# Performance work log

Measured on AMD Instinct MI355X. Metric: run time of the kernel, lower is better.

## Reference

```python
import jax, jax.numpy as jnp
import numpy as np

D_MODEL = 1024
N_HEADS = 16
HEAD_DIM = D_MODEL // N_HEADS
NEG_INF = -1e30


def _rotary(v):
    # v: [B, H, T, hd]. Original module rotates each (even, odd) pair by 90 deg:
    # out[..., 2i] = -v[..., 2i+1]; out[..., 2i+1] = v[..., 2i]
    v2 = v.reshape(*v.shape[:-1], HEAD_DIM // 2, 2)
    return jnp.stack([-v2[..., 1], v2[..., 0]], axis=-1).reshape(v.shape)


def setup_inputs() -> dict:
    key = jax.random.key(0)
    ks = jax.random.split(key, 9)
    B, T, D = 2, 2048, D_MODEL
    s = 1.0 / np.sqrt(D)
    inp = {
        "x": jax.random.normal(ks[0], (B, T, D), dtype=jnp.float32),
        "Wq_w": jax.random.normal(ks[1], (D, D), dtype=jnp.float32) * s,
        "Wq_b": jnp.zeros((D,), dtype=jnp.float32),
        "Wk_w": jax.random.normal(ks[2], (D, D), dtype=jnp.float32) * s,
        "Wk_b": jnp.zeros((D,), dtype=jnp.float32),
        "Wv_w": jax.random.normal(ks[3], (D, D), dtype=jnp.float32) * s,
        "Wv_b": jnp.zeros((D,), dtype=jnp.float32),
        "Wo_w": jax.random.normal(ks[4], (D, D), dtype=jnp.float32) * s,
        "Wo_b": jnp.zeros((D,), dtype=jnp.float32),
    }
    # create_sparse_mask: block-diagonal True windows of size T//4
    window = T // 4
    blk = jnp.arange(T) // window
    inp["sparse_mask"] = blk[:, None] == blk[None, :]
    return inp


def reference(x, Wq_w, Wq_b, Wk_w, Wk_b, Wv_w, Wv_b, Wo_w, Wo_b, sparse_mask):
    B, T, D = x.shape
    H, hd = N_HEADS, HEAD_DIM

    def proj(w, b):  # [B,T,D] -> [B,H,T,hd]
        return (x @ w.T + b).reshape(B, T, H, hd).transpose(0, 2, 1, 3)

    q = _rotary(proj(Wq_w, Wq_b))
    k = _rotary(proj(Wk_w, Wk_b))
    v = proj(Wv_w, Wv_b)

    scores = jnp.einsum("bhqd,bhkd->bhqk", q, k) / jnp.sqrt(jnp.asarray(hd, x.dtype))
    causal = jnp.tril(jnp.ones((T, T), dtype=bool))
    allowed = sparse_mask & causal  # block-diagonal AND causal
    scores = jnp.where(allowed, scores, NEG_INF)
    attn = jax.nn.softmax(scores, axis=-1)  # dropout_p=0.1 omitted (eval mode)
    out = jnp.einsum("bhqk,bhkd->bhqd", attn, v)
    out = out.transpose(0, 2, 1, 3).reshape(B, T, D)
    return out @ Wo_w.T + Wo_b
```

## Files before the change

### kernel.cpp

```cpp
#include <hip/hip_runtime.h>
#include <hip/hip_bf16.h>
#include <stdint.h>

typedef __attribute__((ext_vector_type(4))) float f32x4;
typedef __attribute__((ext_vector_type(8))) __bf16 bf16x8;
typedef __attribute__((ext_vector_type(4))) unsigned short u16x4;
typedef __attribute__((ext_vector_type(8))) unsigned short u16x8;
typedef __attribute__((ext_vector_type(2))) unsigned int u32x2;
typedef const __attribute__((address_space(1))) void* as1_cvp;
typedef __attribute__((address_space(3))) void* as3_vp;

#define LOG2E 1.44269504088896340736f

#define VMW0() asm volatile("s_waitcnt vmcnt(0)" ::: "memory")
#define VMW2() asm volatile("s_waitcnt vmcnt(2)" ::: "memory")
#define VMW4() asm volatile("s_waitcnt vmcnt(4)" ::: "memory")
#define BAR()  do { __builtin_amdgcn_sched_barrier(0); __builtin_amdgcn_s_barrier(); \
                    __builtin_amdgcn_sched_barrier(0); } while (0)

static __device__ __forceinline__ unsigned short f2bf(float f) {
  union { float f; unsigned int u; } c; c.f = f;
  unsigned int r = c.u + 0x7FFFu + ((c.u >> 16) & 1u);
  return (unsigned short)(r >> 16);
}

static __device__ __forceinline__ void gl_lds16(const void* g, void* l) {
  __builtin_amdgcn_global_load_lds((as1_cvp)(uintptr_t)g, (as3_vp)(uintptr_t)l, 16, 0, 0);
}

__global__ __launch_bounds__(256) void cvt_kernel(
    const float* __restrict__ x, const float* __restrict__ wq, const float* __restrict__ wk,
    const float* __restrict__ wv, const float* __restrict__ wo,
    unsigned short* __restrict__ xb, unsigned short* __restrict__ wqb,
    unsigned short* __restrict__ wkb, unsigned short* __restrict__ wvb,
    unsigned short* __restrict__ wob) {
  long e = ((long)blockIdx.x * 256 + threadIdx.x) * 8;
  const float* s; unsigned short* d; long o;
  if (e < 4194304)      { s = x;  d = xb;  o = e; }
  else if (e < 5242880) { s = wq; d = wqb; o = e - 4194304; }
  else if (e < 6291456) { s = wk; d = wkb; o = e - 5242880; }
  else if (e < 7340032) { s = wv; d = wvb; o = e - 6291456; }
  else                  { s = wo; d = wob; o = e - 7340032; }
  float4 a = *(const float4*)(s + o);
  float4 b = *(const float4*)(s + o + 4);
  u16x8 v;
  v[0] = f2bf(a.x); v[1] = f2bf(a.y); v[2] = f2bf(a.z); v[3] = f2bf(a.w);
  v[4] = f2bf(b.x); v[5] = f2bf(b.y); v[6] = f2bf(b.z); v[7] = f2bf(b.w);
  *(u16x8*)(d + o) = v;
}

__global__ __launch_bounds__(512, 2) void gemm_qkv8(
    const unsigned short* __restrict__ xb, const unsigned short* __restrict__ wcat,
    const float* __restrict__ bq, const float* __restrict__ bk, const float* __restrict__ bv,
    unsigned short* __restrict__ qo, unsigned short* __restrict__ ko,
    unsigned short* __restrict__ vto) {
  __shared__ __align__(16) char lds[114688];
  const int tid = threadIdx.x;
  const int lane = tid & 63, wid = tid >> 6;
  const int wm = wid >> 1, wn = wid & 1;
  const int c = lane & 15, g = lane >> 4;

  const int bid = blockIdx.x;
  const int xcd = bid & 7, idx = bid >> 3;
  const int m0 = (((xcd >> 1) << 2) + (idx >> 3)) << 8;
  const int n0 = (((xcd & 1) << 3) + (idx & 7)) * 192;

  const int srow = tid >> 3;
  const int coff = (((tid & 7) ^ (srow & 7)) << 4);
  const char* Ab = (const char*)xb;
  const char* Bb = (const char*)wcat;

  const int swzr0 = ((g ^ (c & 7)) << 4);
  const int swzr1 = (((4 | g) ^ (c & 7)) << 4);

  f32x4 acc[4][6] = {};

  auto STAGE = [&](int kt, int unit) {
    char* db = lds + (kt & 1) * 57344;
    const char* gp; char* dst;
    if (unit < 3) {
      gp = Bb + ((long)(n0 + unit * 64 + srow) << 11) + (kt << 7) + coff;
      dst = db + 32768 + unit * 8192 + tid * 16;
    } else {
      const int u = unit - 3;
      gp = Ab + ((long)(m0 + u * 64 + srow) << 11) + (kt << 7) + coff;
      dst = db + u * 8192 + tid * 16;
    }
    gl_lds16(gp, dst);
  };

#pragma unroll
  for (int uu = 0; uu < 7; ++uu) STAGE(0, uu);
  VMW0();
  BAR();

#pragma unroll 1
  for (int kt = 0; kt < 16; ++kt) {
    const int bufb = (kt & 1) * 57344;
    if (kt < 15) {
#pragma unroll
      for (int uu = 0; uu < 7; ++uu) STAGE(kt + 1, uu);
    }
    bf16x8 aa[4][2];
    const char* pA = lds + bufb + (wm << 13) + (c << 7);
#pragma unroll
    for (int f = 0; f < 4; ++f) {
      aa[f][0] = *(const bf16x8*)(pA + (f << 11) + swzr0);
      aa[f][1] = *(const bf16x8*)(pA + (f << 11) + swzr1);
    }
#pragma unroll
    for (int nf = 0; nf < 6; ++nf) {
      const int rB = wn * 96 + (nf << 4) + c;
      const char* pB = lds + bufb + 32768 + ((rB >> 6) << 13) + ((rB & 63) << 7);
      bf16x8 b0 = *(const bf16x8*)(pB + swzr0);
      bf16x8 b1 = *(const bf16x8*)(pB + swzr1);
      __builtin_amdgcn_s_setprio(1);
#pragma unroll
      for (int f = 0; f < 4; ++f)
        acc[f][nf] = __builtin_amdgcn_mfma_f32_16x16x32_bf16(aa[f][0], b0, acc[f][nf], 0, 0, 0);
#pragma unroll
      for (int f = 0; f < 4; ++f)
        acc[f][nf] = __builtin_amdgcn_mfma_f32_16x16x32_bf16(aa[f][1], b1, acc[f][nf], 0, 0, 0);
      __builtin_amdgcn_s_setprio(0);
    }
    if (kt < 15) VMW0();
    BAR();
  }

#pragma unroll
  for (int nf = 0; nf < 6; ++nf) {
    const int n = n0 + wn * 96 + (nf << 4) + c;
    const int z = n >> 10, nn = n & 1023;
    const float bb_ = (z == 0 ? bq : z == 1 ? bk : bv)[nn];
    const float sc = (z == 0) ? 0.125f : 1.0f;
    const int h = nn >> 6, dd = nn & 63;
#pragma unroll
    for (int a = 0; a < 4; ++a) {
      const int mb = m0 + (wm << 6) + (a << 4) + (g << 2);
      const int b = mb >> 11, tt = mb & 2047;
      if (z < 2) {
        unsigned short* dst = (z == 0 ? qo : ko) +
            ((((long)(b << 4) + h) << 11) + tt) * 64 + dd;
#pragma unroll
        for (int j = 0; j < 4; ++j) dst[(long)j * 64] = f2bf((acc[a][nf][j] + bb_) * sc);
      } else {
        u16x4 pk;
#pragma unroll
        for (int j = 0; j < 4; ++j) pk[j] = f2bf(acc[a][nf][j] + bb_);
        *(u16x4*)(vto + ((((long)((b << 4) + h) << 6) + dd) << 11) + tt) = pk;
      }
    }
  }
}

__global__ __launch_bounds__(512, 2) void gemm_oproj8(
    const unsigned short* __restrict__ ab, const unsigned short* __restrict__ wob,
    const float* __restrict__ bo, float* __restrict__ out) {
  __shared__ __align__(16) char lds[65536];
  const int tid = threadIdx.x;
  const int lane = tid & 63, wid = tid >> 6;
  const int wm = wid >> 2, wn = wid & 3;
  const int c = lane & 15, g = lane >> 4;

  const int bid = blockIdx.x;
  const int swz = (bid & 7) * 32 + (bid >> 3);
  const int n0 = (swz & 7) << 7;
  const int m0 = (swz >> 3) << 7;

  const int srow = tid >> 3;
  const int coff = (((tid & 7) ^ (srow & 7)) << 4);
  const char* Ab = (const char*)ab;
  const char* Bb = (const char*)wob;

  const int swzr0 = ((g ^ (c & 7)) << 4);
  const int swzr1 = (((4 | g) ^ (c & 7)) << 4);

  f32x4 acc[4][2] = {};
  bf16x8 afrA[2][2], afrB[2][2], bbf[2][2];

  auto STAGE = [&](int kt, int unit) {
    char* db = lds + (kt & 1) * 32768;
    const char* gp;
    if (unit < 2) gp = Ab + ((long)(m0 + unit * 64 + srow) << 11) + (kt << 7) + coff;
    else          gp = Bb + ((long)(n0 + (unit - 2) * 64 + srow) << 11) + (kt << 7) + coff;
    gl_lds16(gp, db + unit * 8192 + tid * 16);
  };
  auto RDA = [&](bf16x8 (&dst)[2][2], int bufb, int u) {
    const char* p = lds + bufb + (((u << 6) + (wm << 5) + c) << 7);
#pragma unroll
    for (int f = 0; f < 2; ++f) {
      dst[f][0] = *(const bf16x8*)(p + (f << 11) + swzr0);
      dst[f][1] = *(const bf16x8*)(p + (f << 11) + swzr1);
    }
  };
  auto RDB = [&](int bufb) {
#pragma unroll
    for (int nf = 0; nf < 2; ++nf) {
      const char* p = lds + bufb + 16384 + (((nf << 6) + (wn << 4) + c) << 7);
      bbf[nf][0] = *(const bf16x8*)(p + swzr0);
      bbf[nf][1] = *(const bf16x8*)(p + swzr1);
    }
  };
  auto MM = [&](int u, const bf16x8 (&af)[2][2]) {
    __builtin_amdgcn_s_setprio(1);
#pragma unroll
    for (int f = 0; f < 2; ++f)
#pragma unroll
      for (int nf = 0; nf < 2; ++nf)
#pragma unroll
        for (int kf = 0; kf < 2; ++kf)
          acc[u * 2 + f][nf] = __builtin_amdgcn_mfma_f32_16x16x32_bf16(
              af[f][kf], bbf[nf][kf], acc[u * 2 + f][nf], 0, 0, 0);
    __builtin_amdgcn_s_setprio(0);
  };

  STAGE(0, 0); STAGE(0, 2); STAGE(0, 3); STAGE(0, 1);

#pragma unroll 1
  for (int kt = 0; kt < 15; ++kt) {
    const int bufb = (kt & 1) * 32768;
    STAGE(kt + 1, 0); STAGE(kt + 1, 2);
    VMW2(); BAR();
    RDB(bufb); RDA(afrA, bufb, 0); RDA(afrB, bufb, 1);
    MM(0, afrA);
    STAGE(kt + 1, 3); STAGE(kt + 1, 1);
    BAR();
    MM(1, afrB);
  }
  {
    VMW0(); BAR();
    RDB(32768); RDA(afrA, 32768, 0); RDA(afrB, 32768, 1);
    MM(0, afrA);
    MM(1, afrB);
  }

#pragma unroll
  for (int nf = 0; nf < 2; ++nf) {
    const int n = n0 + (nf << 6) + (wn << 4) + c;
    const float bb = bo[n];
#pragma unroll
    for (int a = 0; a < 4; ++a) {
      const int mb = m0 + ((a >> 1) << 6) + (wm << 5) + ((a & 1) << 4) + (g << 2);
#pragma unroll
      for (int j = 0; j < 4; ++j)
        out[((long)(mb + j) << 10) + n] = acc[a][nf][j] + bb;
    }
  }
}

__global__ __launch_bounds__(512) void attn_kernel(
    const unsigned short* __restrict__ qg, const unsigned short* __restrict__ kg,
    const unsigned short* __restrict__ vtg, unsigned short* __restrict__ og) {
  __shared__ __align__(16) char kv_s[3][16384];
  __shared__ __align__(16) char p_s[8][2304];

  const int bx = blockIdx.x, bh = blockIdx.y;
  const int map1[16] = {3,7,11,15, 2,6,10,14, 0,4,8,12, 1,5,9,13};
  const int map2[16] = {0,4,8,12, 1,5,9,13, 3,7,11,15, 2,6,10,14};
  const int qt = (bh < 16) ? map1[bx] : map2[bx];
  const int tid = threadIdx.x;
  const int lane = tid & 63, w = tid >> 6;
  const int c = lane & 15, g = lane >> 4;
  const int q0 = qt << 7;
  const int wstart = q0 & ~511;
  const int nt = ((q0 - wstart) >> 6) + 2;

  const unsigned short* qrow = qg + (((long)bh << 11) + q0 + (w << 4) + c) * 64;
  bf16x8 qa0 = *(const bf16x8*)(qrow + (g << 3));
  bf16x8 qa1 = *(const bf16x8*)(qrow + (g << 3) + 32);

  float m_run = -3.0e38f, l_run = 0.0f;
  f32x4 oacc[4] = {};

  const int sr = tid >> 3;
  const int jx16 = (((tid & 7) ^ (sr & 7)) << 4);
  const char* kbase = (const char*)kg + ((((long)bh << 11) + sr) << 7) + jx16;
  const char* vbase = (const char*)vtg + ((((long)bh << 6) + sr) << 12) + jx16;
  const int t16 = tid << 4;

  auto STAGEKV = [&](int kv0, int bsel) {
    char* dst = kv_s[bsel];
    gl_lds16(kbase + ((long)kv0 << 7), dst + t16);
    gl_lds16(vbase + ((long)kv0 << 1), dst + 8192 + t16);
  };

  STAGEKV(wstart, 0);
  STAGEKV(wstart + 64, 1);

  int rsel = 0, ssel = 2;
  for (int t = 0; t < nt; ++t) {
    if (t + 2 < nt) {
      STAGEKV(wstart + ((t + 2) << 6), ssel);
      VMW4();
    } else if (t + 1 < nt) {
      VMW2();
    } else {
      VMW0();
    }
    BAR();

    const char* kb_ = kv_s[rsel];
    const char* vb_ = kv_s[rsel] + 8192;
    const int kv0 = wstart + (t << 6);

    f32x4 sacc[4] = {};
    __builtin_amdgcn_s_setprio(1);
#pragma unroll
    for (int mf = 0; mf < 4; ++mf) {
      const int kr = (mf << 4) + c;
      const char* kp = kb_ + (kr << 7);
      bf16x8 k0 = *(const bf16x8*)(kp + ((g ^ (kr & 7)) << 4));
      bf16x8 k1 = *(const bf16x8*)(kp + (((4 | g) ^ (kr & 7)) << 4));
      sacc[mf] = __builtin_amdgcn_mfma_f32_16x16x32_bf16(k0, qa0, sacc[mf], 0, 0, 0);
      sacc[mf] = __builtin_amdgcn_mfma_f32_16x16x32_bf16(k1, qa1, sacc[mf], 0, 0, 0);
    }
    __builtin_amdgcn_s_setprio(0);

    const int dkv = kv0 - q0;
    if (dkv > (w << 4) - 64) {
      const int qrel = (w << 4) + c;
#pragma unroll
      for (int mf = 0; mf < 4; ++mf)
#pragma unroll
        for (int j = 0; j < 4; ++j)
          if (dkv + (mf << 4) + (g << 2) + j > qrel) sacc[mf][j] = -3.0e38f;
    }

    float pm[4];
#pragma unroll
    for (int mf = 0; mf < 4; ++mf)
      pm[mf] = fmaxf(fmaxf(sacc[mf][0], sacc[mf][1]), fmaxf(sacc[mf][2], sacc[mf][3]));
    float pmax = fmaxf(fmaxf(pm[0], pm[1]), fmaxf(pm[2], pm[3]));
    pmax = fmaxf(pmax, __shfl_xor(pmax, 16));
    pmax = fmaxf(pmax, __shfl_xor(pmax, 32));

    const bool resc = !__all(pmax <= m_run + 8.0f);
    const float m_new = resc ? fmaxf(m_run, pmax) : m_run;

    const float mL = m_new * LOG2E;
    float ls[4];
#pragma unroll
    for (int mf = 0; mf < 4; ++mf) {
      float p0 = __builtin_amdgcn_exp2f(__builtin_fmaf(sacc[mf][0], LOG2E, -mL));
      float p1 = __builtin_amdgcn_exp2f(__builtin_fmaf(sacc[mf][1], LOG2E, -mL));
      float p2 = __builtin_amdgcn_exp2f(__builtin_fmaf(sacc[mf][2], LOG2E, -mL));
      float p3 = __builtin_amdgcn_exp2f(__builtin_fmaf(sacc[mf][3], LOG2E, -mL));
      sacc[mf][0] = p0; sacc[mf][1] = p1; sacc[mf][2] = p2; sacc[mf][3] = p3;
      ls[mf] = (p0 + p1) + (p2 + p3);
    }
    float lsum = (ls[0] + ls[1]) + (ls[2] + ls[3]);
    lsum += __shfl_xor(lsum, 16);
    lsum += __shfl_xor(lsum, 32);

    if (resc) {
      const float alpha = __builtin_amdgcn_exp2f((m_run - m_new) * LOG2E);
      l_run *= alpha;
#pragma unroll
      for (int j = 0; j < 4; ++j) {
        const float aj = __shfl(alpha, (g << 2) + j);
#pragma unroll
        for (int nf = 0; nf < 4; ++nf) oacc[nf][j] *= aj;
      }
      m_run = m_new;
    }
    l_run += lsum;

    {
      char* pw = p_s[w] + c * 144;
#pragma unroll
      for (int mf = 0; mf < 4; ++mf) {
        unsigned int p01, p23;
        asm("v_cvt_pk_bf16_f32 %0, %1, %2" : "=v"(p01) : "v"(sacc[mf][0]), "v"(sacc[mf][1]));
        asm("v_cvt_pk_bf16_f32 %0, %1, %2" : "=v"(p23) : "v"(sacc[mf][2]), "v"(sacc[mf][3]));
        u32x2 pk; pk[0] = p01; pk[1] = p23;
        *(u32x2*)(pw + (mf << 5) + (g << 3)) = pk;
      }
    }

    const char* pr = p_s[w] + c * 144;
    __builtin_amdgcn_s_setprio(1);
#pragma unroll
    for (int kk = 0; kk < 2; ++kk) {
      bf16x8 pa = *(const bf16x8*)(pr + (kk << 6) + (g << 4));
#pragma unroll
      for (int nf = 0; nf < 4; ++nf) {
        const int vr = (nf << 4) + c;
        bf16x8 vb = *(const bf16x8*)(vb_ + (vr << 7) +
                                     ((((kk << 2) | g) ^ (vr & 7)) << 4));
        oacc[nf] = __builtin_amdgcn_mfma_f32_16x16x32_bf16(pa, vb, oacc[nf], 0, 0, 0);
      }
    }
    __builtin_amdgcn_s_setprio(0);
    BAR();

    rsel = (rsel == 2) ? 0 : rsel + 1;
    ssel = (ssel == 2) ? 0 : ssel + 1;
  }

  const int b = bh >> 4, h = bh & 15;
#pragma unroll
  for (int j = 0; j < 4; ++j) {
    const float linv = 1.0f / __shfl(l_run, (g << 2) + j);
    const int trow = q0 + (w << 4) + (g << 2) + j;
    unsigned short* dst = og + ((((long)(b << 11)) + trow) << 10) + (h << 6);
#pragma unroll
    for (int nf = 0; nf < 4; ++nf)
      dst[(nf << 4) + c] = f2bf(oacc[nf][j] * linv);
  }
}

extern "C" void kernel_launch(void* const* d_in, const int* in_sizes, int n_in,
                              void* d_out, int out_size, void* d_ws, size_t ws_size,
                              hipStream_t stream) {
  const float* x  = (const float*)d_in[0];
  const float* wq = (const float*)d_in[1];
  const float* bq = (const float*)d_in[2];
  const float* wk = (const float*)d_in[3];
  const float* bk = (const float*)d_in[4];
  const float* wv = (const float*)d_in[5];
  const float* bv = (const float*)d_in[6];
  const float* wo = (const float*)d_in[7];
  const float* bo = (const float*)d_in[8];

  char* ws = (char*)d_ws;
  unsigned short* xb    = (unsigned short*)(ws);
  unsigned short* wqb   = (unsigned short*)(ws + 8388608);
  unsigned short* wkb   = (unsigned short*)(ws + 10485760);
  unsigned short* wvb   = (unsigned short*)(ws + 12582912);
  unsigned short* wob   = (unsigned short*)(ws + 14680064);
  unsigned short* qb    = (unsigned short*)(ws + 16777216);
  unsigned short* kb    = (unsigned short*)(ws + 25165824);
  unsigned short* vtb   = (unsigned short*)(ws + 33554432);
  unsigned short* attnb = xb;

  cvt_kernel<<<4096, 256, 0, stream>>>(x, wq, wk, wv, wo, xb, wqb, wkb, wvb, wob);
  gemm_qkv8<<<256, 512, 0, stream>>>(xb, wqb, bq, bk, bv, qb, kb, vtb);
  attn_kernel<<<dim3(16, 32), 512, 0, stream>>>(qb, kb, vtb, attnb);
  gemm_oproj8<<<256, 512, 0, stream>>>(attnb, wob, bo, (float*)d_out);
}
```

Measured before the change: 77.98 us.

## Halve GEMM tile sizes to double grid size and raise occupancy

Both the QKV and output-projection GEMMs shrink their M tile (256→128 and 128→64 rows), so each launches 512 blocks instead of 256 and uses less LDS with fewer accumulators, allowing four blocks per CU. The output projection also drops its split-stage software pipeline in favor of the simpler double-buffered loop used by the QKV kernel, and both get new XCD-aware block-to-tile mappings. The aim is to fill all CUs better on a small problem. The cost is less data reuse per block (more global/LDS traffic per FLOP) and the loss of the finer-grained overlap in oproj.

Result: faster. 72.38 us (-7.2%).

```diff
diff --git a/kernel.cpp b/kernel.cpp
--- a/kernel.cpp
+++ b/kernel.cpp
@@ -49,20 +49,20 @@
   *(u16x8*)(d + o) = v;
 }
 
-__global__ __launch_bounds__(512, 2) void gemm_qkv8(
+__global__ __launch_bounds__(512, 4) void gemm_qkv8(
     const unsigned short* __restrict__ xb, const unsigned short* __restrict__ wcat,
     const float* __restrict__ bq, const float* __restrict__ bk, const float* __restrict__ bv,
     unsigned short* __restrict__ qo, unsigned short* __restrict__ ko,
     unsigned short* __restrict__ vto) {
-  __shared__ __align__(16) char lds[114688];
+  __shared__ __align__(16) char lds[81920];
   const int tid = threadIdx.x;
   const int lane = tid & 63, wid = tid >> 6;
-  const int wm = wid >> 1, wn = wid & 1;
+  const int wm = wid >> 2, wn = wid & 3;
   const int c = lane & 15, g = lane >> 4;
 
   const int bid = blockIdx.x;
   const int xcd = bid & 7, idx = bid >> 3;
-  const int m0 = (((xcd >> 1) << 2) + (idx >> 3)) << 8;
+  const int m0 = (((xcd >> 1) << 3) + (idx >> 3)) << 7;
   const int n0 = (((xcd & 1) << 3) + (idx & 7)) * 192;
 
   const int srow = tid >> 3;
@@ -73,33 +73,32 @@
   const int swzr0 = ((g ^ (c & 7)) << 4);
   const int swzr1 = (((4 | g) ^ (c & 7)) << 4);
 
-  f32x4 acc[4][6] = {};
+  f32x4 acc[4][3] = {};
 
   auto STAGE = [&](int kt, int unit) {
-    char* db = lds + (kt & 1) * 57344;
+    char* db = lds + (kt & 1) * 40960;
     const char* gp; char* dst;
-    if (unit < 3) {
-      gp = Bb + ((long)(n0 + unit * 64 + srow) << 11) + (kt << 7) + coff;
-      dst = db + 32768 + unit * 8192 + tid * 16;
+    if (unit < 2) {
+      gp = Ab + ((long)(m0 + unit * 64 + srow) << 11) + (kt << 7) + coff;
+      dst = db + unit * 8192 + tid * 16;
     } else {
-      const int u = unit - 3;
-      gp = Ab + ((long)(m0 + u * 64 + srow) << 11) + (kt << 7) + coff;
-      dst = db + u * 8192 + tid * 16;
+      gp = Bb + ((long)(n0 + (unit - 2) * 64 + srow) << 11) + (kt << 7) + coff;
+      dst = db + 16384 + (unit - 2) * 8192 + tid * 16;
     }
     gl_lds16(gp, dst);
   };
 
 #pragma unroll
-  for (int uu = 0; uu < 7; ++uu) STAGE(0, uu);
+  for (int uu = 0; uu < 5; ++uu) STAGE(0, uu);
   VMW0();
   BAR();
 
 #pragma unroll 1
   for (int kt = 0; kt < 16; ++kt) {
-    const int bufb = (kt & 1) * 57344;
+    const int bufb = (kt & 1) * 40960;
     if (kt < 15) {
 #pragma unroll
-      for (int uu = 0; uu < 7; ++uu) STAGE(kt + 1, uu);
+      for (int uu = 0; uu < 5; ++uu) STAGE(kt + 1, uu);
     }
     bf16x8 aa[4][2];
     const char* pA = lds + bufb + (wm << 13) + (c << 7);
@@ -109,9 +108,9 @@
       aa[f][1] = *(const bf16x8*)(pA + (f << 11) + swzr1);
     }
 #pragma unroll
-    for (int nf = 0; nf < 6; ++nf) {
-      const int rB = wn * 96 + (nf << 4) + c;
-      const char* pB = lds + bufb + 32768 + ((rB >> 6) << 13) + ((rB & 63) << 7);
+    for (int nf = 0; nf < 3; ++nf) {
+      const int rB = wn * 48 + (nf << 4) + c;
+      const char* pB = lds + bufb + 16384 + ((rB >> 6) << 13) + ((rB & 63) << 7);
       bf16x8 b0 = *(const bf16x8*)(pB + swzr0);
       bf16x8 b1 = *(const bf16x8*)(pB + swzr1);
       __builtin_amdgcn_s_setprio(1);
@@ -128,8 +127,8 @@
   }
 
 #pragma unroll
-  for (int nf = 0; nf < 6; ++nf) {
-    const int n = n0 + wn * 96 + (nf << 4) + c;
+  for (int nf = 0; nf < 3; ++nf) {
+    const int n = n0 + wn * 48 + (nf << 4) + c;
     const int z = n >> 10, nn = n & 1023;
     const float bb_ = (z == 0 ? bq : z == 1 ? bk : bv)[nn];
     const float sc = (z == 0) ? 0.125f : 1.0f;
@@ -153,19 +152,19 @@
   }
 }
 
-__global__ __launch_bounds__(512, 2) void gemm_oproj8(
+__global__ __launch_bounds__(512, 4) void gemm_oproj8(
     const unsigned short* __restrict__ ab, const unsigned short* __restrict__ wob,
     const float* __restrict__ bo, float* __restrict__ out) {
-  __shared__ __align__(16) char lds[65536];
+  __shared__ __align__(16) char lds[49152];
   const int tid = threadIdx.x;
   const int lane = tid & 63, wid = tid >> 6;
   const int wm = wid >> 2, wn = wid & 3;
   const int c = lane & 15, g = lane >> 4;
 
   const int bid = blockIdx.x;
-  const int swz = (bid & 7) * 32 + (bid >> 3);
-  const int n0 = (swz & 7) << 7;
-  const int m0 = (swz >> 3) << 7;
+  const int xcd = bid & 7, idx = bid >> 3;
+  const int m0 = ((xcd << 3) + (idx >> 3)) << 6;
+  const int n0 = (idx & 7) << 7;
 
   const int srow = tid >> 3;
   const int coff = (((tid & 7) ^ (srow & 7)) << 4);
@@ -175,75 +174,65 @@
   const int swzr0 = ((g ^ (c & 7)) << 4);
   const int swzr1 = (((4 | g) ^ (c & 7)) << 4);
 
-  f32x4 acc[4][2] = {};
-  bf16x8 afrA[2][2], afrB[2][2], bbf[2][2];
+  f32x4 acc[2][2] = {};
 
   auto STAGE = [&](int kt, int unit) {
-    char* db = lds + (kt & 1) * 32768;
-    const char* gp;
-    if (unit < 2) gp = Ab + ((long)(m0 + unit * 64 + srow) << 11) + (kt << 7) + coff;
-    else          gp = Bb + ((long)(n0 + (unit - 2) * 64 + srow) << 11) + (kt << 7) + coff;
-    gl_lds16(gp, db + unit * 8192 + tid * 16);
+    char* db = lds + (kt & 1) * 24576;
+    const char* gp; char* dst;
+    if (unit == 0) {
+      gp = Ab + ((long)(m0 + srow) << 11) + (kt << 7) + coff;
+      dst = db + tid * 16;
+    } else {
+      gp = Bb + ((long)(n0 + (unit - 1) * 64 + srow) << 11) + (kt << 7) + coff;
+      dst = db + unit * 8192 + tid * 16;
+    }
+    gl_lds16(gp, dst);
   };
-  auto RDA = [&](bf16x8 (&dst)[2][2], int bufb, int u) {
-    const char* p = lds + bufb + (((u << 6) + (wm << 5) + c) << 7);
+
+  STAGE(0, 0); STAGE(0, 1); STAGE(0, 2);
+  VMW0();
+  BAR();
+
+#pragma unroll 1
+  for (int kt = 0; kt < 16; ++kt) {
+    const int bufb = (kt & 1) * 24576;
+    if (kt < 15) { STAGE(kt + 1, 0); STAGE(kt + 1, 1); STAGE(kt + 1, 2); }
+    bf16x8 aa[2][2];
+    const char* pA = lds + bufb + (wm << 12) + (c << 7);
 #pragma unroll
     for (int f = 0; f < 2; ++f) {
-      dst[f][0] = *(const bf16x8*)(p + (f << 11) + swzr0);
-      dst[f][1] = *(const bf16x8*)(p + (f << 11) + swzr1);
-    }
-  };
-  auto RDB = [&](int bufb) {
+      aa[f][0] = *(const bf16x8*)(pA + (f << 11) + swzr0);
+      aa[f][1] = *(const bf16x8*)(pA + (f << 11) + swzr1);
+    }
 #pragma unroll
     for (int nf = 0; nf < 2; ++nf) {
-      const char* p = lds + bufb + 16384 + (((nf << 6) + (wn << 4) + c) << 7);
-      bbf[nf][0] = *(const bf16x8*)(p + swzr0);
-      bbf[nf][1] = *(const bf16x8*)(p + swzr1);
-    }
-  };
-  auto MM = [&](int u, const bf16x8 (&af)[2][2]) {
-    __builtin_amdgcn_s_setprio(1);
-#pragma unroll
-    for (int f = 0; f < 2; ++f)
-#pragma unroll
-      for (int nf = 0; nf < 2; ++nf)
-#pragma unroll
-        for (int kf = 0; kf < 2; ++kf)
-          acc[u * 2 + f][nf] = __builtin_amdgcn_mfma_f32_16x16x32_bf16(
-              af[f][kf], bbf[nf][kf], acc[u * 2 + f][nf], 0, 0, 0);
-    __builtin_amdgcn_s_setprio(0);
-  };
-
-  STAGE(0, 0); STAGE(0, 2); STAGE(0, 3); STAGE(0, 1);
-
-#pragma unroll 1
-  for (int kt = 0; kt < 15; ++kt) {
-    const int bufb = (kt & 1) * 32768;
-    STAGE(kt + 1, 0); STAGE(kt + 1, 2);
-    VMW2(); BAR();
-    RDB(bufb); RDA(afrA, bufb, 0); RDA(afrB, bufb, 1);
-    MM(0, afrA);
-    STAGE(kt + 1, 3); STAGE(kt + 1, 1);
+      const int rB = (wn << 5) + (nf << 4) + c;
+      const char* pB = lds + bufb + 8192 + ((rB >> 6) << 13) + ((rB & 63) << 7);
+      bf16x8 b0 = *(const bf16x8*)(pB + swzr0);
+      bf16x8 b1 = *(const bf16x8*)(pB + swzr1);
+      __builtin_amdgcn_s_setprio(1);
+#pragma unroll
+      for (int f = 0; f < 2; ++f)
+        acc[f][nf] = __builtin_amdgcn_mfma_f32_16x16x32_bf16(aa[f][0], b0, acc[f][nf], 0, 0, 0);
+#pragma unroll
+      for (int f = 0; f < 2; ++f)
+        acc[f][nf] = __builtin_amdgcn_mfma_f32_16x16x32_bf16(aa[f][1], b1, acc[f][nf], 0, 0, 0);
+      __builtin_amdgcn_s_setprio(0);
+    }
+    if (kt < 15) VMW0();
     BAR();
-    MM(1, afrB);
-  }
-  {
-    VMW0(); BAR();
-    RDB(32768); RDA(afrA, 32768, 0); RDA(afrB, 32768, 1);
-    MM(0, afrA);
-    MM(1, afrB);
   }
 
 #pragma unroll
   for (int nf = 0; nf < 2; ++nf) {
-    const int n = n0 + (nf << 6) + (wn << 4) + c;
+    const int n = n0 + (wn << 5) + (nf << 4) + c;
     const float bb = bo[n];
 #pragma unroll
-    for (int a = 0; a < 4; ++a) {
-      const int mb = m0 + ((a >> 1) << 6) + (wm << 5) + ((a & 1) << 4) + (g << 2);
+    for (int f = 0; f < 2; ++f) {
+      const int mb = m0 + (wm << 5) + (f << 4) + (g << 2);
 #pragma unroll
       for (int j = 0; j < 4; ++j)
-        out[((long)(mb + j) << 10) + n] = acc[a][nf][j] + bb;
+        out[((long)(mb + j) << 10) + n] = acc[f][nf][j] + bb;
     }
   }
 }
@@ -434,7 +423,7 @@
   unsigned short* attnb = xb;
 
   cvt_kernel<<<4096, 256, 0, stream>>>(x, wq, wk, wv, wo, xb, wqb, wkb, wvb, wob);
-  gemm_qkv8<<<256, 512, 0, stream>>>(xb, wqb, bq, bk, bv, qb, kb, vtb);
+  gemm_qkv8<<<512, 512, 0, stream>>>(xb, wqb, bq, bk, bv, qb, kb, vtb);
   attn_kernel<<<dim3(16, 32), 512, 0, stream>>>(qb, kb, vtb, attnb);
-  gemm_oproj8<<<256, 512, 0, stream>>>(attnb, wob, bo, (float*)d_out);
-}
+  gemm_oproj8<<<512, 512, 0, stream>>>(attnb, wob, bo, (float*)d_out);
+}
```
